# Kernel tuning notes

Measured on AMD Instinct MI355X. Metric: run time of the kernel, lower is better.

The kernel has to match this reference:

```python
import jax, jax.numpy as jnp
import numpy as np

U = 2048
D = 2048
N_HEADS = 16
D_HEAD = D // N_HEADS
FFN_MULT = 4
D_FF = FFN_MULT * D
EPS = 1e-6


def _rmsnorm(x, w):
    # x: [U, D], w: [D]
    ms = jnp.mean(jnp.square(x), axis=-1, keepdims=True)
    return x * jax.lax.rsqrt(ms + EPS) * w


def setup_inputs() -> dict:
    key = jax.random.key(0)
    ks = jax.random.split(key, 12)
    d = {}
    d["x"] = jax.random.normal(ks[0], (U, D), dtype=jnp.float32)
    d["adj_bias"] = jax.random.normal(ks[1], (U, U), dtype=jnp.float32)
    # learned params (torch nn.Linear stores weight as [out, in]; y = x @ W.T)
    init = lambda k, shape, std: jax.random.normal(k, shape, dtype=jnp.float32) * std
    d["norm1_w"] = jnp.ones((D,), dtype=jnp.float32)
    d["norm2_w"] = jnp.ones((D,), dtype=jnp.float32)
    d["wq"] = init(ks[2], (D, D), (1.0 / D) ** 0.5)
    d["wk"] = init(ks[3], (D, D), (1.0 / D) ** 0.5)
    d["wv"] = init(ks[4], (D, D), (1.0 / D) ** 0.5)
    d["wo"] = init(ks[5], (D, D), (2.0 / D) ** 0.5)  # nn.init.normal_ std=(2/D)^0.5
    d["w_up"] = init(ks[6], (D_FF, D), (1.0 / D) ** 0.5)
    d["b_up"] = jnp.zeros((D_FF,), dtype=jnp.float32)
    d["w_down"] = init(ks[7], (D, D_FF), (2.0 / D_FF) ** 0.5)
    d["b_down"] = jnp.zeros((D,), dtype=jnp.float32)
    return d


def reference(x, adj_bias, norm1_w, norm2_w, wq, wk, wv, wo, w_up, b_up, w_down, b_down):
    scale = 1.0 / (D_HEAD ** 0.5)
    h = _rmsnorm(x, norm1_w)
    # project and split heads: [U, D] -> [H, U, d]
    q = (h @ wq.T).reshape(U, N_HEADS, D_HEAD).transpose(1, 0, 2)
    k = (h @ wk.T).reshape(U, N_HEADS, D_HEAD).transpose(1, 0, 2)
    v = (h @ wv.T).reshape(U, N_HEADS, D_HEAD).transpose(1, 0, 2)
    scores = jnp.einsum('hud,hvd->huv', q, k) * scale + adj_bias[None, :, :]
    attn = jax.nn.softmax(scores, axis=-1)
    out = jnp.einsum('huv,hvd->hud', attn, v)  # [H, U, d]
    out = out.transpose(1, 0, 2).reshape(U, D)
    x = x + out @ wo.T
    h2 = _rmsnorm(x, norm2_w)
    ff = jax.nn.gelu(h2 @ w_up.T + b_up, approximate=False)
    x = x + ff @ w_down.T + b_down
    return x
```

## Files before the change

kernel.cpp:

```cpp
#include <hip/hip_runtime.h>
#include <hip/hip_fp16.h>
#include <cstdint>
#include <cstddef>

#define U_DIM 2048
#define D_DIM 2048
#define NH 16
#define DH 128
#define DFF 8192
#define EPS_RMS 1e-6f
#define ATTN_SCALE 0.088388347648318447f

typedef unsigned short u16;
typedef __attribute__((ext_vector_type(4))) float floatx4;
typedef __attribute__((ext_vector_type(8))) short shortx8;

__device__ __forceinline__ float bf2f(u16 u) {
  union { unsigned int i; float f; } v; v.i = ((unsigned int)u) << 16; return v.f;
}
__device__ __forceinline__ u16 f2bf(float f) {
  union { float f; unsigned int i; } v; v.f = f;
  return (u16)((v.i + 0x7fffu + ((v.i >> 16) & 1u)) >> 16);
}
__device__ __forceinline__ u16 f2h(float f) {
  __half h = __float2half_rn(f);
  union { __half h; u16 u; } c; c.h = h; return c.u;
}
__device__ __forceinline__ float h2f(u16 u) {
  union { __half h; u16 u; } c; c.u = u; return __half2float(c.h);
}

__device__ __forceinline__ void f2b_body(const float* __restrict__ in,
                                         u16* __restrict__ out, int i, int n4) {
  if (i >= n4) return;
  float4 f = reinterpret_cast<const float4*>(in)[i];
  ushort4 o;
  o.x = f2bf(f.x); o.y = f2bf(f.y); o.z = f2bf(f.z); o.w = f2bf(f.w);
  reinterpret_cast<ushort4*>(out)[i] = o;
}

__global__ __launch_bounds__(256) void k_f2b4(
    const float* __restrict__ s0, const float* __restrict__ s1,
    const float* __restrict__ s2, const float* __restrict__ s3,
    u16* __restrict__ d0, u16* __restrict__ d1,
    u16* __restrict__ d2, u16* __restrict__ d3, int n4) {
  const float* s; u16* d;
  switch (blockIdx.y) {
    case 0: s = s0; d = d0; break;
    case 1: s = s1; d = d1; break;
    case 2: s = s2; d = d2; break;
    default: s = s3; d = d3; break;
  }
  f2b_body(s, d, blockIdx.x * 256 + threadIdx.x, n4);
}

__global__ __launch_bounds__(256) void k_f2b2(
    const float* __restrict__ s0, const float* __restrict__ s1,
    u16* __restrict__ d0, u16* __restrict__ d1, int n4) {
  const float* s = blockIdx.y ? s1 : s0;
  u16* d = blockIdx.y ? d1 : d0;
  f2b_body(s, d, blockIdx.x * 256 + threadIdx.x, n4);
}

__global__ __launch_bounds__(256) void k_prep_bias(const float* __restrict__ adj,
                                                   u16* __restrict__ adjp) {
  const int tile = blockIdx.x;
  const int qt = tile >> 4, kt = tile & 15;
  const int t = threadIdx.x;
  const int c16 = t & 15, rblk = t >> 4;
  u16* outt = adjp + (size_t)tile * 16384;
#pragma unroll
  for (int rr = 0; rr < 8; rr++) {
    int r = rblk * 8 + rr;
    const float* src = adj + (size_t)(qt * 128 + r) * U_DIM + kt * 128 + c16;
    ushort4 o0, o1;
    o0.x = f2h(src[0]);    o0.y = f2h(src[16]);  o0.z = f2h(src[32]);  o0.w = f2h(src[48]);
    o1.x = f2h(src[64]);   o1.y = f2h(src[80]);  o1.z = f2h(src[96]);  o1.w = f2h(src[112]);
    ushort4* dst = reinterpret_cast<ushort4*>(outt + ((size_t)c16 * 128 + r) * 8);
    dst[0] = o0; dst[1] = o1;
  }
}

__global__ __launch_bounds__(256) void k_reduce4(
    const u16* __restrict__ p0, const u16* __restrict__ p1,
    const u16* __restrict__ p2, const u16* __restrict__ p3,
    const float* __restrict__ X, const float* __restrict__ bias,
    float* __restrict__ out, int n4) {
  int i = blockIdx.x * 256 + threadIdx.x;
  if (i >= n4) return;
  ushort4 a = reinterpret_cast<const ushort4*>(p0)[i];
  ushort4 b = reinterpret_cast<const ushort4*>(p1)[i];
  ushort4 c = reinterpret_cast<const ushort4*>(p2)[i];
  ushort4 d = reinterpret_cast<const ushort4*>(p3)[i];
  float4 xv = reinterpret_cast<const float4*>(X)[i];
  float4 r;
  r.x = xv.x + bf2f(a.x) + bf2f(b.x) + bf2f(c.x) + bf2f(d.x);
  r.y = xv.y + bf2f(a.y) + bf2f(b.y) + bf2f(c.y) + bf2f(d.y);
  r.z = xv.z + bf2f(a.z) + bf2f(b.z) + bf2f(c.z) + bf2f(d.z);
  r.w = xv.w + bf2f(a.w) + bf2f(b.w) + bf2f(c.w) + bf2f(d.w);
  if (bias) {
    int col = (i * 4) & (D_DIM - 1);
    float4 bv = *reinterpret_cast<const float4*>(bias + col);
    r.x += bv.x; r.y += bv.y; r.z += bv.z; r.w += bv.w;
  }
  reinterpret_cast<float4*>(out)[i] = r;
}

__global__ __launch_bounds__(256) void k_reduce4norm(
    const u16* __restrict__ p0, const u16* __restrict__ p1,
    const u16* __restrict__ p2, const u16* __restrict__ p3,
    const float* __restrict__ X, const float* __restrict__ w,
    float* __restrict__ out, u16* __restrict__ nrm) {
  const int row = blockIdx.x;
  const int t = threadIdx.x;
  const size_t base = (size_t)row * 512;
  float4 r[2];
  float ss = 0.f;
#pragma unroll
  for (int h = 0; h < 2; h++) {
    size_t i = base + t + h * 256;
    ushort4 a = reinterpret_cast<const ushort4*>(p0)[i];
    ushort4 b = reinterpret_cast<const ushort4*>(p1)[i];
    ushort4 c = reinterpret_cast<const ushort4*>(p2)[i];
    ushort4 d = reinterpret_cast<const ushort4*>(p3)[i];
    float4 xv = reinterpret_cast<const float4*>(X)[i];
    float4 v;
    v.x = xv.x + bf2f(a.x) + bf2f(b.x) + bf2f(c.x) + bf2f(d.x);
    v.y = xv.y + bf2f(a.y) + bf2f(b.y) + bf2f(c.y) + bf2f(d.y);
    v.z = xv.z + bf2f(a.z) + bf2f(b.z) + bf2f(c.z) + bf2f(d.z);
    v.w = xv.w + bf2f(a.w) + bf2f(b.w) + bf2f(c.w) + bf2f(d.w);
    reinterpret_cast<float4*>(out)[i] = v;
    ss += v.x*v.x + v.y*v.y + v.z*v.z + v.w*v.w;
    r[h] = v;
  }
#pragma unroll
  for (int off = 32; off > 0; off >>= 1) ss += __shfl_xor(ss, off);
  __shared__ float red[4];
  if ((t & 63) == 0) red[t >> 6] = ss;
  __syncthreads();
  float tot = red[0] + red[1] + red[2] + red[3];
  float rms = rsqrtf(tot / (float)D_DIM + EPS_RMS);
  const float4* wr = reinterpret_cast<const float4*>(w);
#pragma unroll
  for (int h = 0; h < 2; h++) {
    float4 wv = wr[t + h * 256];
    ushort4 o;
    o.x = f2bf(r[h].x * rms * wv.x); o.y = f2bf(r[h].y * rms * wv.y);
    o.z = f2bf(r[h].z * rms * wv.z); o.w = f2bf(r[h].w * rms * wv.w);
    reinterpret_cast<ushort4*>(nrm)[base + t + h * 256] = o;
  }
}

__global__ __launch_bounds__(256) void k_rmsnorm(const float* __restrict__ x,
                                                 const float* __restrict__ w,
                                                 u16* __restrict__ out) {
  const int row = blockIdx.x;
  const int t = threadIdx.x;
  const float4* xr = reinterpret_cast<const float4*>(x + (size_t)row * D_DIM);
  float4 a0 = xr[t], a1 = xr[t + 256];
  float ss = a0.x*a0.x + a0.y*a0.y + a0.z*a0.z + a0.w*a0.w
           + a1.x*a1.x + a1.y*a1.y + a1.z*a1.z + a1.w*a1.w;
#pragma unroll
  for (int off = 32; off > 0; off >>= 1) ss += __shfl_xor(ss, off);
  __shared__ float red[4];
  if ((t & 63) == 0) red[t >> 6] = ss;
  __syncthreads();
  float tot = red[0] + red[1] + red[2] + red[3];
  float r = rsqrtf(tot / (float)D_DIM + EPS_RMS);
  const float4* wr = reinterpret_cast<const float4*>(w);
  float4 w0 = wr[t], w1 = wr[t + 256];
  ushort4 o0, o1;
  o0.x = f2bf(a0.x * r * w0.x); o0.y = f2bf(a0.y * r * w0.y);
  o0.z = f2bf(a0.z * r * w0.z); o0.w = f2bf(a0.w * r * w0.w);
  o1.x = f2bf(a1.x * r * w1.x); o1.y = f2bf(a1.y * r * w1.y);
  o1.z = f2bf(a1.z * r * w1.z); o1.w = f2bf(a1.w * r * w1.w);
  ushort4* op = reinterpret_cast<ushort4*>(out + (size_t)row * D_DIM);
  op[t] = o0; op[t + 256] = o1;
}

__device__ __forceinline__ void async16(u16* lds, const u16* g) {
  __builtin_amdgcn_global_load_lds(
      (__attribute__((address_space(1))) void*)(g),
      (__attribute__((address_space(3))) void*)(lds), 16, 0, 0);
}

#define BK64 64

__device__ __forceinline__ void gemm256_core(
    const u16* __restrict__ A, int lda,
    const u16* __restrict__ B, int ldb,
    int K, int bm, int bn, u16* smem, floatx4 acc[8][4]) {
  const int t = threadIdx.x;
  const int wv = t >> 6, lane = t & 63;
  const int wm = wv >> 2, wn = wv & 3;
  const int fr = lane & 15, kq = lane >> 4;
  const int srow = wv * 8 + (lane >> 3);
  const int scg  = (lane & 7) ^ (lane >> 3);
  const u16* Ag = A + (size_t)(bm + srow) * lda + scg * 8;
  const u16* Bg = B + (size_t)(bn + srow) * ldb + scg * 8;
  u16* AsW = smem + (wv * 8) * 64;
  u16* BsW = smem + 32768 + (wv * 8) * 64;
  const int swz  = fr & 7;
  const int arow = wm * 128 + fr;
  const int brow = wn * 64 + fr;
  const int nt = K / BK64;
#pragma unroll
  for (int r = 0; r < 4; r++) async16(AsW + r * 4096, Ag + (size_t)(r * 64) * lda);
#pragma unroll
  for (int r = 0; r < 4; r++) async16(BsW + r * 4096, Bg + (size_t)(r * 64) * ldb);
  int cur = 0;
  for (int kt = 0; kt < nt; kt++) {
    asm volatile("s_waitcnt vmcnt(0) lgkmcnt(0)" ::: "memory");
    __builtin_amdgcn_sched_barrier(0);
    __builtin_amdgcn_s_barrier();
    __builtin_amdgcn_sched_barrier(0);
    asm volatile("" ::: "memory");
    if (kt + 1 < nt) {
      const int nb = (cur ^ 1) * 16384;
      const size_t ko = (size_t)(kt + 1) * BK64;
#pragma unroll
      for (int r = 0; r < 4; r++) async16(AsW + nb + r * 4096, Ag + (size_t)(r * 64) * lda + ko);
#pragma unroll
      for (int r = 0; r < 4; r++) async16(BsW + nb + r * 4096, Bg + (size_t)(r * 64) * ldb + ko);
    }
    const u16* Ab = smem + cur * 16384;
    const u16* Bb = smem + 32768 + cur * 16384;
#pragma unroll
    for (int ksub = 0; ksub < 2; ksub++) {
      const int cswz = (((ksub * 4 + kq) ^ swz) * 8);
      shortx8 bfr[4];
#pragma unroll
      for (int j = 0; j < 4; j++)
        bfr[j] = *reinterpret_cast<const shortx8*>(Bb + (brow + j * 16) * 64 + cswz);
#pragma unroll
      for (int mi = 0; mi < 8; mi++) {
        shortx8 afr = *reinterpret_cast<const shortx8*>(Ab + (arow + mi * 16) * 64 + cswz);
#pragma unroll
        for (int j = 0; j < 4; j++)
          acc[mi][j] = __builtin_amdgcn_mfma_f32_16x16x32_bf16(afr, bfr[j], acc[mi][j], 0, 0, 0);
      }
    }
    cur ^= 1;
  }
}

#define GEMM256_PRELUDE                                           \
  __shared__ u16 smem[65536];                         \
  floatx4 acc[8][4];                                              \
  {                                                               \
    floatx4 zf = {0.f, 0.f, 0.f, 0.f};                            \
    for (int i = 0; i < 8; i++)                                   \
      for (int j = 0; j < 4; j++) acc[i][j] = zf;                 \
  }                                                               \
  const int bm = blockIdx.y * 256, bn = blockIdx.x * 256;

#define EPILOG256                                                 \
  const int lane_ = threadIdx.x & 63;                             \
  const int wv_ = threadIdx.x >> 6;                               \
  const int fr_ = lane_ & 15, kq_ = lane_ >> 4;                   \
  const int row0 = (wv_ >> 2) * 128 + kq_ * 4;                    \
  const int col0 = (wv_ & 3) * 64 + fr_;

__global__ __launch_bounds__(512, 1) void k_gemm_qkv(
    const u16* __restrict__ A, const u16* __restrict__ B,
    u16* __restrict__ Q, u16* __restrict__ Ko, u16* __restrict__ VT) {
  GEMM256_PRELUDE;
  gemm256_core(A, D_DIM, B, D_DIM, D_DIM, bm, bn, smem, acc);
  EPILOG256;
  if (bn < 4096) {
    u16* C = (bn < 2048) ? Q : Ko;
    const int cb = (bn < 2048) ? bn : bn - 2048;
#pragma unroll
    for (int mt = 0; mt < 8; mt++)
#pragma unroll
      for (int i = 0; i < 4; i++) {
        u16* cr = C + (size_t)(bm + row0 + mt*16 + i) * D_DIM + cb + col0;
#pragma unroll
        for (int nt = 0; nt < 4; nt++) cr[nt*16] = f2bf(acc[mt][nt][i]);
      }
  } else {
    const int cb = bn - 4096;
#pragma unroll
    for (int mt = 0; mt < 8; mt++)
#pragma unroll
      for (int nt = 0; nt < 4; nt++) {
        int col = cb + col0 + nt*16;
        int row = bm + row0 + mt*16;
        ushort4 o;
        o.x = f2bf(acc[mt][nt][0]); o.y = f2bf(acc[mt][nt][1]);
        o.z = f2bf(acc[mt][nt][2]); o.w = f2bf(acc[mt][nt][3]);
        *reinterpret_cast<ushort4*>(VT + (size_t)col * U_DIM + row) = o;
      }
  }
}

__global__ __launch_bounds__(512, 1) void k_gemm_splitk_part(
    const u16* __restrict__ A, int lda, const u16* __restrict__ B, int ldb,
    int Kc, u16* __restrict__ P, size_t pstride, int ldc) {
  GEMM256_PRELUDE;
  const int koff = blockIdx.z * Kc;
  gemm256_core(A + koff, lda, B + koff, ldb, Kc, bm, bn, smem, acc);
  u16* Pz = P + (size_t)blockIdx.z * pstride;
  EPILOG256;
#pragma unroll
  for (int mt = 0; mt < 8; mt++)
#pragma unroll
    for (int i = 0; i < 4; i++) {
      u16* cr = Pz + (size_t)(bm + row0 + mt*16 + i) * ldc + bn + col0;
#pragma unroll
      for (int nt = 0; nt < 4; nt++) cr[nt*16] = f2bf(acc[mt][nt][i]);
    }
}

__device__ __forceinline__ float fast_gelu(float v) {
  float u = v * (0.79788456080286536f + 0.035677408136300125f * v * v);
  float tt = fminf(fmaxf(2.f * u, -40.f), 40.f);
  float e = __expf(tt);
  return 0.5f * v * (1.f + (e - 1.f) / (e + 1.f));
}

__global__ __launch_bounds__(512, 1) void k_gemm_gelu(
    const u16* __restrict__ A, int lda, const u16* __restrict__ B, int ldb,
    int K, const float* __restrict__ bias, u16* __restrict__ C, int ldc) {
  GEMM256_PRELUDE;
  gemm256_core(A, lda, B, ldb, K, bm, bn, smem, acc);
  EPILOG256;
#pragma unroll
  for (int mt = 0; mt < 8; mt++)
#pragma unroll
    for (int i = 0; i < 4; i++) {
      size_t off = (size_t)(bm + row0 + mt*16 + i) * ldc + bn + col0;
#pragma unroll
      for (int nt = 0; nt < 4; nt++) {
        float v = acc[mt][nt][i] + bias[bn + col0 + nt*16];
        C[off + nt*16] = f2bf(fast_gelu(v));
      }
    }
}

__global__ __launch_bounds__(256) void k_flash(
    const u16* __restrict__ Q, const u16* __restrict__ K,
    const u16* __restrict__ VT, const u16* __restrict__ ADJP,
    u16* __restrict__ O) {
  __shared__ u16 smem[36864];
  const int qt = blockIdx.x, gh = blockIdx.y;
  const int t = threadIdx.x, wv = t >> 6, lane = t & 63;
  const int fr = lane & 15, kq = lane >> 4;
  const int c4 = lane & 3, r4 = lane >> 2;

  const u16* gq = Q + (size_t)(qt * 64) * D_DIM + gh * DH;
  const u16* gk = K + gh * DH;
  const u16* gv = VT + (size_t)(gh * DH) * U_DIM;

#pragma unroll
  for (int it = 0; it < 4; it++) {
    int row = wv * 16 + it * 4 + kq;
    int cg = (fr + row) & 15;
    async16(smem + row * 128 + fr * 8, gq + (size_t)row * D_DIM + cg * 8);
  }
  __builtin_amdgcn_s_waitcnt(0);
  __syncthreads();
  shortx8 qf[4];
#pragma unroll
  for (int ks = 0; ks < 4; ks++) {
    int row = wv * 16 + fr;
    int slot = ((ks * 4 + kq) - row) & 15;
    qf[ks] = *reinterpret_cast<const shortx8*>(smem + row * 128 + slot * 8);
  }
  __syncthreads();

  floatx4 oacc[8];
  float lrow[4];
#pragma unroll
  for (int nt = 0; nt < 8; nt++) { floatx4 z = {0.f,0.f,0.f,0.f}; oacc[nt] = z; }
#pragma unroll
  for (int i = 0; i < 4; i++) lrow[i] = 0.f;

  {
    u16* Ks = smem; u16* Vs = smem + 16384;
#pragma unroll
    for (int it = 0; it < 4; it++) {
      int row = wv * 16 + it * 4 + kq;
      int cg = (fr + row) & 15;
      async16(Ks + row * 128 + fr * 8, gk + (size_t)row * D_DIM + cg * 8);
    }
#pragma unroll
    for (int sub = 0; sub < 2; sub++)
#pragma unroll
      for (int it = 0; it < 2; it++) {
        int row = wv * 32 + it * 16 + r4;
        int cg = (c4 + (row >> 1)) & 3;
        async16(Vs + sub * 4096 + row * 32 + c4 * 8,
                gv + (size_t)row * U_DIM + sub * 32 + cg * 8);
      }
  }

  u16* Pb = smem + 32768;
  for (int kt64 = 0; kt64 < 32; kt64++) {
    const int cur = kt64 & 1;
    u16* Ks = smem + cur * 8192;
    u16* Vs = smem + 16384 + cur * 8192;
    asm volatile("s_waitcnt vmcnt(0)" ::: "memory");
    __builtin_amdgcn_s_barrier();
    asm volatile("" ::: "memory");
    if (kt64 < 31) {
      u16* Kn = smem + (1 - cur) * 8192;
      u16* Vn = smem + 16384 + (1 - cur) * 8192;
      const u16* gkn = gk + (size_t)((kt64 + 1) * 64) * D_DIM;
      const u16* gvn = gv + (kt64 + 1) * 64;
#pragma unroll
      for (int it = 0; it < 4; it++) {
        int row = wv * 16 + it * 4 + kq;
        int cg = (fr + row) & 15;
        async16(Kn + row * 128 + fr * 8, gkn + (size_t)row * D_DIM + cg * 8);
      }
#pragma unroll
      for (int sub = 0; sub < 2; sub++)
#pragma unroll
        for (int it = 0; it < 2; it++) {
          int row = wv * 32 + it * 16 + r4;
          int cg = (c4 + (row >> 1)) & 3;
          async16(Vn + sub * 4096 + row * 32 + c4 * 8,
                  gvn + (size_t)row * U_DIM + sub * 32 + cg * 8);
        }
    }

    floatx4 sacc[4];
    { floatx4 z = {0.f,0.f,0.f,0.f}; sacc[0]=z; sacc[1]=z; sacc[2]=z; sacc[3]=z; }
#pragma unroll
    for (int ks = 0; ks < 4; ks++) {
      int slotA = ((ks * 4 + kq) - fr) & 15;
      int slotB = ((ks * 4 + kq) - (16 + fr)) & 15;
      shortx8 kf0 = *reinterpret_cast<const shortx8*>(Ks + fr * 128 + slotA * 8);
      shortx8 kf1 = *reinterpret_cast<const shortx8*>(Ks + (16 + fr) * 128 + slotB * 8);
      shortx8 kf2 = *reinterpret_cast<const shortx8*>(Ks + (32 + fr) * 128 + slotA * 8);
      shortx8 kf3 = *reinterpret_cast<const shortx8*>(Ks + (48 + fr) * 128 + slotB * 8);
      sacc[0] = __builtin_amdgcn_mfma_f32_16x16x32_bf16(qf[ks], kf0, sacc[0], 0, 0, 0);
      sacc[1] = __builtin_amdgcn_mfma_f32_16x16x32_bf16(qf[ks], kf1, sacc[1], 0, 0, 0);
      sacc[2] = __builtin_amdgcn_mfma_f32_16x16x32_bf16(qf[ks], kf2, sacc[2], 0, 0, 0);
      sacc[3] = __builtin_amdgcn_mfma_f32_16x16x32_bf16(qf[ks], kf3, sacc[3], 0, 0, 0);
    }

    const u16* bt = ADJP + ((size_t)(qt >> 1) * 16 + (kt64 >> 1)) * 16384 + (kt64 & 1) * 4;
#pragma unroll
    for (int i = 0; i < 4; i++) {
      int rl = wv * 16 + kq * 4 + i;
      int r128 = (qt & 1) * 64 + rl;
      ushort4 bh = *reinterpret_cast<const ushort4*>(bt + ((size_t)fr * 128 + r128) * 8);
      float s0 = sacc[0][i] * ATTN_SCALE + h2f(bh.x);
      float s1 = sacc[1][i] * ATTN_SCALE + h2f(bh.y);
      float s2 = sacc[2][i] * ATTN_SCALE + h2f(bh.z);
      float s3 = sacc[3][i] * ATTN_SCALE + h2f(bh.w);
      float p0 = __expf(fminf(s0, 80.f));
      float p1 = __expf(fminf(s1, 80.f));
      float p2 = __expf(fminf(s2, 80.f));
      float p3 = __expf(fminf(s3, 80.f));
      int slot0 = ((fr >> 3) - (rl >> 1)) & 3;
      int slot1 = (((16 + fr) >> 3) - (rl >> 1)) & 3;
      Pb[rl * 64 + slot0 * 8 + (fr & 7)] = f2bf(p0);
      Pb[rl * 64 + slot1 * 8 + (fr & 7)] = f2bf(p1);
      Pb[rl * 64 + 32 + slot0 * 8 + (fr & 7)] = f2bf(p2);
      Pb[rl * 64 + 32 + slot1 * 8 + (fr & 7)] = f2bf(p3);
      lrow[i] += (p0 + p1) + (p2 + p3);
    }
    asm volatile("s_waitcnt lgkmcnt(0)" ::: "memory");
    __builtin_amdgcn_s_barrier();
    asm volatile("" ::: "memory");

    shortx8 pf0, pf1;
    {
      int row = wv * 16 + fr;
      int slot = (kq - (row >> 1)) & 3;
      pf0 = *reinterpret_cast<const shortx8*>(Pb + row * 64 + slot * 8);
      pf1 = *reinterpret_cast<const shortx8*>(Pb + row * 64 + 32 + slot * 8);
    }
#pragma unroll
    for (int nt = 0; nt < 8; nt++) {
      int row = nt * 16 + fr;
      int slot = (kq - (row >> 1)) & 3;
      shortx8 vf0 = *reinterpret_cast<const shortx8*>(Vs + row * 32 + slot * 8);
      shortx8 vf1 = *reinterpret_cast<const shortx8*>(Vs + 4096 + row * 32 + slot * 8);
      oacc[nt] = __builtin_amdgcn_mfma_f32_16x16x32_bf16(pf0, vf0, oacc[nt], 0, 0, 0);
      oacc[nt] = __builtin_amdgcn_mfma_f32_16x16x32_bf16(pf1, vf1, oacc[nt], 0, 0, 0);
    }
  }

#pragma unroll
  for (int i = 0; i < 4; i++) {
    int rl = wv * 16 + kq * 4 + i;
    float l = lrow[i];
    l += __shfl_xor(l, 1);
    l += __shfl_xor(l, 2);
    l += __shfl_xor(l, 4);
    l += __shfl_xor(l, 8);
    float inv = 1.f / l;
    u16* orow = O + (size_t)(qt * 64 + rl) * D_DIM + gh * DH + fr;
#pragma unroll
    for (int nt = 0; nt < 8; nt++)
      orow[nt * 16] = f2bf(oacc[nt][i] * inv);
  }
}

extern "C" void kernel_launch(void* const* d_in, const int* in_sizes, int n_in,
                              void* d_out, int out_size, void* d_ws, size_t ws_size,
                              hipStream_t stream) {
  (void)in_sizes; (void)n_in; (void)out_size; (void)ws_size;
  const float* x      = (const float*)d_in[0];
  const float* adj    = (const float*)d_in[1];
  const float* n1w    = (const float*)d_in[2];
  const float* n2w    = (const float*)d_in[3];
  const float* wq     = (const float*)d_in[4];
  const float* wk     = (const float*)d_in[5];
  const float* wv     = (const float*)d_in[6];
  const float* wo     = (const float*)d_in[7];
  const float* w_up   = (const float*)d_in[8];
  const float* b_up   = (const float*)d_in[9];
  const float* w_down = (const float*)d_in[10];
  const float* b_down = (const float*)d_in[11];
  float* out = (float*)d_out;
  char* ws = (char*)d_ws;
  const size_t MB = 1u << 20;
  u16* hb   = (u16*)(ws + 0*MB);
  u16* qb   = (u16*)(ws + 8*MB);
  u16* kb   = (u16*)(ws + 16*MB);
  u16* vtb  = (u16*)(ws + 24*MB);
  u16* adjp = (u16*)(ws + 32*MB);
  u16* aob  = (u16*)(ws + 40*MB);
  u16* wob  = (u16*)(ws + 48*MB);
  u16* wqkv = (u16*)(ws + 56*MB);
  u16* opp  = (u16*)(ws + 8*MB);
  u16* h2b  = (u16*)(ws + 0*MB);
  u16* wub  = (u16*)(ws + 8*MB);
  u16* ffb  = (u16*)(ws + 40*MB);
  u16* wdb  = (u16*)(ws + 72*MB);
  u16* dpp  = (u16*)(ws + 8*MB);

  dim3 blk(256);
  dim3 blk512(512);
  const int n4d = (D_DIM * D_DIM) / 4;
  const int n4f = (DFF * D_DIM) / 4;
  const size_t szd = (size_t)D_DIM * D_DIM;

  k_f2b4<<<dim3((n4d + 255) / 256, 4), blk, 0, stream>>>(
      wq, wk, wv, wo, wqkv, wqkv + szd, wqkv + 2*szd, wob, n4d);
  k_prep_bias<<<256, blk, 0, stream>>>(adj, adjp);
  k_rmsnorm<<<U_DIM, blk, 0, stream>>>(x, n1w, hb);

  k_gemm_qkv<<<dim3(24, 8), blk512, 0, stream>>>(hb, wqkv, qb, kb, vtb);

  k_flash<<<dim3(32, 16), blk, 0, stream>>>(qb, kb, vtb, adjp, aob);

  k_gemm_splitk_part<<<dim3(8, 8, 4), blk512, 0, stream>>>(
      aob, D_DIM, wob, D_DIM, D_DIM/4, opp, szd, D_DIM);
  k_reduce4norm<<<U_DIM, blk, 0, stream>>>(
      opp, opp + szd, opp + 2*szd, opp + 3*szd, x, n2w, out, h2b);

  k_f2b2<<<dim3((n4f + 255) / 256, 2), blk, 0, stream>>>(w_up, w_down, wub, wdb, n4f);
  k_gemm_gelu<<<dim3(32, 8), blk512, 0, stream>>>(h2b, D_DIM, wub, D_DIM, D_DIM,
                                                  b_up, ffb, DFF);
  k_gemm_splitk_part<<<dim3(8, 8, 4), blk512, 0, stream>>>(
      ffb, DFF, wdb, DFF, DFF/4, dpp, szd, D_DIM);
  k_reduce4<<<(n4d + 255) / 256, blk, 0, stream>>>(
      dpp, dpp + szd, dpp + 2*szd, dpp + 3*szd, out, b_down, out, n4d);
}
```

Baseline: 532.7 us.

## Use exp2 softmax with pre-scaled fp16 bias, fp16 P/V, drop barrier

The adjacency-bias prep kernel now pre-multiplies the bias by log2(e) and shifts it by -4. The attention kernel folds log2(e) into the score scale and uses the hardware exp2 builtin instead of __expf, which saves a multiply per score. P and the transposed V are now stored in fp16 and the PV MFMA uses the f16 variant, giving more mantissa bits in exchange for a smaller range; the -4 shift and a clamp at 14 are meant to keep P within fp16. The workgroup barrier between writing P to LDS and reading it back is removed on the assumption that each wave only reads its own rows, which risks a race if that assumption is wrong.

```diff
diff --git a/kernel.cpp b/kernel.cpp
--- a/kernel.cpp
+++ b/kernel.cpp
@@ -10,6 +10,8 @@
 #define DFF 8192
 #define EPS_RMS 1e-6f
 #define ATTN_SCALE 0.088388347648318447f
+#define LOG2E 1.4426950408889634f
+#define ATTN_SCALE2 (ATTN_SCALE * LOG2E)
 
 typedef unsigned short u16;
 typedef __attribute__((ext_vector_type(4))) float floatx4;
@@ -74,8 +76,10 @@
     int r = rblk * 8 + rr;
     const float* src = adj + (size_t)(qt * 128 + r) * U_DIM + kt * 128 + c16;
     ushort4 o0, o1;
-    o0.x = f2h(src[0]);    o0.y = f2h(src[16]);  o0.z = f2h(src[32]);  o0.w = f2h(src[48]);
-    o1.x = f2h(src[64]);   o1.y = f2h(src[80]);  o1.z = f2h(src[96]);  o1.w = f2h(src[112]);
+    o0.x = f2h(src[0]   * LOG2E - 4.f); o0.y = f2h(src[16]  * LOG2E - 4.f);
+    o0.z = f2h(src[32]  * LOG2E - 4.f); o0.w = f2h(src[48]  * LOG2E - 4.f);
+    o1.x = f2h(src[64]  * LOG2E - 4.f); o1.y = f2h(src[80]  * LOG2E - 4.f);
+    o1.z = f2h(src[96]  * LOG2E - 4.f); o1.w = f2h(src[112] * LOG2E - 4.f);
     ushort4* dst = reinterpret_cast<ushort4*>(outt + ((size_t)c16 * 128 + r) * 8);
     dst[0] = o0; dst[1] = o1;
   }
@@ -287,8 +291,8 @@
         int col = cb + col0 + nt*16;
         int row = bm + row0 + mt*16;
         ushort4 o;
-        o.x = f2bf(acc[mt][nt][0]); o.y = f2bf(acc[mt][nt][1]);
-        o.z = f2bf(acc[mt][nt][2]); o.w = f2bf(acc[mt][nt][3]);
+        o.x = f2h(acc[mt][nt][0]); o.y = f2h(acc[mt][nt][1]);
+        o.z = f2h(acc[mt][nt][2]); o.w = f2h(acc[mt][nt][3]);
         *reinterpret_cast<ushort4*>(VT + (size_t)col * U_DIM + row) = o;
       }
   }
@@ -447,25 +451,22 @@
       int rl = wv * 16 + kq * 4 + i;
       int r128 = (qt & 1) * 64 + rl;
       ushort4 bh = *reinterpret_cast<const ushort4*>(bt + ((size_t)fr * 128 + r128) * 8);
-      float s0 = sacc[0][i] * ATTN_SCALE + h2f(bh.x);
-      float s1 = sacc[1][i] * ATTN_SCALE + h2f(bh.y);
-      float s2 = sacc[2][i] * ATTN_SCALE + h2f(bh.z);
-      float s3 = sacc[3][i] * ATTN_SCALE + h2f(bh.w);
-      float p0 = __expf(fminf(s0, 80.f));
-      float p1 = __expf(fminf(s1, 80.f));
-      float p2 = __expf(fminf(s2, 80.f));
-      float p3 = __expf(fminf(s3, 80.f));
+      float s0 = sacc[0][i] * ATTN_SCALE2 + h2f(bh.x);
+      float s1 = sacc[1][i] * ATTN_SCALE2 + h2f(bh.y);
+      float s2 = sacc[2][i] * ATTN_SCALE2 + h2f(bh.z);
+      float s3 = sacc[3][i] * ATTN_SCALE2 + h2f(bh.w);
+      float p0 = __builtin_amdgcn_exp2f(fminf(s0, 14.f));
+      float p1 = __builtin_amdgcn_exp2f(fminf(s1, 14.f));
+      float p2 = __builtin_amdgcn_exp2f(fminf(s2, 14.f));
+      float p3 = __builtin_amdgcn_exp2f(fminf(s3, 14.f));
       int slot0 = ((fr >> 3) - (rl >> 1)) & 3;
       int slot1 = (((16 + fr) >> 3) - (rl >> 1)) & 3;
-      Pb[rl * 64 + slot0 * 8 + (fr & 7)] = f2bf(p0);
-      Pb[rl * 64 + slot1 * 8 + (fr & 7)] = f2bf(p1);
-      Pb[rl * 64 + 32 + slot0 * 8 + (fr & 7)] = f2bf(p2);
-      Pb[rl * 64 + 32 + slot1 * 8 + (fr & 7)] = f2bf(p3);
+      Pb[rl * 64 + slot0 * 8 + (fr & 7)] = f2h(p0);
+      Pb[rl * 64 + slot1 * 8 + (fr & 7)] = f2h(p1);
+      Pb[rl * 64 + 32 + slot0 * 8 + (fr & 7)] = f2h(p2);
+      Pb[rl * 64 + 32 + slot1 * 8 + (fr & 7)] = f2h(p3);
       lrow[i] += (p0 + p1) + (p2 + p3);
     }
-    asm volatile("s_waitcnt lgkmcnt(0)" ::: "memory");
-    __builtin_amdgcn_s_barrier();
-    asm volatile("" ::: "memory");
 
     shortx8 pf0, pf1;
     {
@@ -480,8 +481,8 @@
       int slot = (kq - (row >> 1)) & 3;
       shortx8 vf0 = *reinterpret_cast<const shortx8*>(Vs + row * 32 + slot * 8);
       shortx8 vf1 = *reinterpret_cast<const shortx8*>(Vs + 4096 + row * 32 + slot * 8);
-      oacc[nt] = __builtin_amdgcn_mfma_f32_16x16x32_bf16(pf0, vf0, oacc[nt], 0, 0, 0);
-      oacc[nt] = __builtin_amdgcn_mfma_f32_16x16x32_bf16(pf1, vf1, oacc[nt], 0, 0, 0);
+      oacc[nt] = __builtin_amdgcn_mfma_f32_16x16x32_f16(pf0, vf0, oacc[nt], 0, 0, 0);
+      oacc[nt] = __builtin_amdgcn_mfma_f32_16x16x32_f16(pf1, vf1, oacc[nt], 0, 0, 0);
     }
   }
 
```

Result: no change. 542.2 us (+1.8%).
